# Optimization experiments

Hardware: AMD Instinct MI355X
Metric: run time of the kernel (lower is better)

Reference implementation:

```python
import jax, jax.numpy as jnp
import numpy as np


def setup_inputs() -> dict:
    key = jax.random.key(0)
    ks = jax.random.split(key, 15)
    B, r, d, h, na = 64, 64, 2048, 64, 256
    x = jax.random.normal(ks[0], (B, d, na), dtype=jnp.float32)
    L = jax.random.randint(ks[1], (B, 2, na), 0, 2).astype(jnp.float32)
    p = lambda i, shp: jax.random.normal(ks[i], shp, dtype=jnp.float32)
    return {
        "x": x, "L": L,
        "Aq": p(2, (r, d)), "Ak": p(3, (r, d)), "Av": p(4, (r, d)),
        "Aq1": p(5, (r, r)), "Ak1": p(6, (r, r)), "Av1": p(7, (r, r)),
        "Aq5": p(8, (r, r)), "Ak5": p(9, (r, r)), "Av5": p(10, (r, r)),
        "Ao": p(11, (r, r)), "Ao1": p(12, (r, r)), "Ao5": p(13, (h, r)),
    }


def reference(x, L, Aq, Ak, Av, Aq1, Ak1, Av1, Aq5, Ak5, Av5, Ao, Ao1, Ao5):
    B, d, na = x.shape
    # numNeighbors: count of L[:,0,:] >= 1 per batch, +1 -> [B,1,1]
    numN = jnp.sum((L[:, 0, :] >= 1.0).astype(jnp.float32), axis=1)[:, None, None] + 1.0
    scale = jnp.sqrt(numN)  # [B,1,1]

    def attn(M, Wq, Wk, Wv):
        # M: [B, f, na]; Wq/Wk/Wv: [r, f]
        Q = jax.nn.sigmoid(jnp.einsum('rf,bfn->bnr', Wq, M))  # [B,na,r]
        K = jax.nn.sigmoid(jnp.einsum('rf,bfn->brn', Wk, M))  # [B,r,na]
        V = jax.nn.sigmoid(jnp.einsum('rf,bfn->bnr', Wv, M))  # [B,na,r]
        A = jax.nn.softmax(jnp.einsum('bnr,brm->bnm', Q, K) / scale, axis=2)
        return jnp.einsum('bnm,bmr->brn', A, V)  # [B,r,na]

    o = attn(x, Aq, Ak, Av)
    M = jax.nn.silu(jnp.einsum('sr,brn->bsn', Ao, o))
    o = attn(M, Aq1, Ak1, Av1)
    M = jax.nn.silu(jnp.einsum('sr,brn->bsn', Ao1, o))
    o = attn(M, Aq5, Ak5, Av5)
    M = jax.nn.silu(jnp.einsum('hr,brn->bhn', Ao5, o))  # [B,h,na]

    blk = d // na  # rows per block (8)
    def diagvec(i):
        # kron(sum-of-squares, ones(1,2)) == repeat each element twice -> [B, 2*na]
        return jnp.repeat(jnp.sum(M[:, i * blk:(i + 1) * blk, :] ** 2, axis=1), 2, axis=1)

    M11, M12, M21, M22 = diagvec(0), diagvec(1), diagvec(2), diagvec(3)
    Mpp = jnp.sum(M[:, 4 * blk:, :] ** 2, axis=1)  # [B, na]

    # q = x[:, :4, :].transpose(1,2).reshape(B, 4*na) (agent-major ordering)
    q = jnp.transpose(x[:, :4, :], (0, 2, 1)).reshape(B, 4 * na)
    q1, q2 = q[:, :2 * na], q[:, 2 * na:]
    # Block matrix [[diag(M11), diag(M12)], [diag(M21), diag(M22)]] quadratic form,
    # computed without materializing the [B, 4na, 4na] matrix.
    quad = jnp.sum(M11 * q1 * q1 + M12 * q1 * q2 + M21 * q2 * q1 + M22 * q2 * q2,
                   axis=1, keepdims=True)
    return quad + jnp.sum(Mpp, axis=1, keepdims=True)  # [B, 1]
```

## Files before the change

kernel.cpp:

```cpp
#include <hip/hip_runtime.h>
#include <stdint.h>

typedef _Float16 f16;
typedef f16 f16x8 __attribute__((ext_vector_type(8)));
typedef float f32x4 __attribute__((ext_vector_type(4)));

#define MFMA(a,b,c) __builtin_amdgcn_mfma_f32_16x16x32_f16(a, b, c, 0, 0, 0)

__device__ __forceinline__ float sigmoidf_(float z) {
  return __builtin_amdgcn_rcpf(1.0f + __expf(-z));
}

__global__ void prep_kernel(const float* __restrict__ L,
    const float* __restrict__ Aq, const float* __restrict__ Ak, const float* __restrict__ Av,
    const float* __restrict__ Aq1, const float* __restrict__ Ak1, const float* __restrict__ Av1,
    const float* __restrict__ Aq5, const float* __restrict__ Ak5, const float* __restrict__ Av5,
    const float* __restrict__ Ao, const float* __restrict__ Ao1, const float* __restrict__ Ao5,
    float* __restrict__ scale, f16* __restrict__ Wcat, f16* __restrict__ Wsm,
    float* __restrict__ out)
{
  __shared__ float r4[4];
  int blk = blockIdx.x, t = threadIdx.x;
  if (blk < 64) {
    float v = (L[blk * 512 + t] >= 1.0f) ? 1.0f : 0.0f;
    #pragma unroll
    for (int off = 32; off; off >>= 1) v += __shfl_down(v, off);
    if ((t & 63) == 0) r4[t >> 6] = v;
    __syncthreads();
    if (t == 0) scale[blk] = sqrtf(r4[0] + r4[1] + r4[2] + r4[3] + 1.0f);
  } else if (blk < 160) {
    int base = (blk - 64) * 4096;
    for (int i = 0; i < 16; i++) {
      int idx = base + t + i * 256;
      int row = idx >> 11, col = idx & 2047;
      float v = (row < 64) ? Aq[row * 2048 + col]
              : (row < 128) ? Ak[(row - 64) * 2048 + col]
              : Av[(row - 128) * 2048 + col];
      Wcat[idx] = (f16)v;
    }
  } else if (blk < 169) {
    int j = blk - 160;
    const float* s = (j == 0) ? Aq1 : (j == 1) ? Ak1 : (j == 2) ? Av1 : (j == 3) ? Aq5
                   : (j == 4) ? Ak5 : (j == 5) ? Av5 : (j == 6) ? Ao : (j == 7) ? Ao1 : Ao5;
    for (int i = 0; i < 16; i++) { int idx = t + i * 256; Wsm[j * 4096 + idx] = (f16)s[idx]; }
  } else {
    if (t < 64) out[t] = 0.0f;
  }
}

__global__ __launch_bounds__(256, 4) void qkv1_kernel(const float* __restrict__ x,
    const f16* __restrict__ Wcat, f16* __restrict__ Qt, f16* __restrict__ Kt,
    f16* __restrict__ Vg)
{
  int rs = blockIdx.x, b = blockIdx.y, ng = blockIdx.z;
  int n0 = ng * 32, rbase = rs * 64;
  int t = threadIdx.x, lane = t & 63, w = t >> 6;
  int l15 = lane & 15, q = lane >> 4;
  __shared__ f16 xt[2][32 * 72];
  __shared__ f16 wt[2][64 * 72];
  f32x4 acc[2] = {};
  const float* xb = x + (size_t)b * 524288 + n0;
  int tn = t & 31, fg = t >> 5;

  int r0 = t >> 3,          c0 = t & 7;
  int r1 = (t + 256) >> 3,  c1 = (t + 256) & 7;
  const f16* pw0 = Wcat + (size_t)(rbase + r0) * 2048 + c0 * 8;
  const f16* pw1 = Wcat + (size_t)(rbase + r1) * 2048 + c1 * 8;
  const float* px = xb + (size_t)(fg * 8) * 256 + tn;

  float xa0, xa1, xa2, xa3, xa4, xa5, xa6, xa7;
  uint4 wr0, wr1;

#define LOAD_X(f0n) do {                                                        \
    const float* xp_ = px + (size_t)(f0n) * 256;                                \
    xa0 = xp_[0];    xa1 = xp_[256];  xa2 = xp_[512];  xa3 = xp_[768];          \
    xa4 = xp_[1024]; xa5 = xp_[1280]; xa6 = xp_[1536]; xa7 = xp_[1792];         \
  } while (0)

#define LOAD_W(f0n) do {                                                        \
    wr0 = *(const uint4*)(pw0 + (f0n)); wr1 = *(const uint4*)(pw1 + (f0n));     \
  } while (0)

#define WRITE_XW(buf) do {                                                      \
    f16x8 pk_;                                                                  \
    pk_[0] = (f16)xa0; pk_[1] = (f16)xa1; pk_[2] = (f16)xa2; pk_[3] = (f16)xa3; \
    pk_[4] = (f16)xa4; pk_[5] = (f16)xa5; pk_[6] = (f16)xa6; pk_[7] = (f16)xa7; \
    *(f16x8*)&xt[buf][tn * 72 + fg * 8] = pk_;                                  \
    f16* wb_ = &wt[buf][0];                                                     \
    *(uint4*)&wb_[r0 * 72 + c0 * 8] = wr0;                                      \
    *(uint4*)&wb_[r1 * 72 + c1 * 8] = wr1;                                      \
  } while (0)

  LOAD_X(0);
  LOAD_W(0);
  WRITE_XW(0);
  __syncthreads();

  int cur = 0;
  for (int f0 = 0; f0 < 2048; f0 += 64) {
    int nxt = cur ^ 1;
    bool more = (f0 + 64 < 2048);
    if (more) { LOAD_X(f0 + 64); LOAD_W(f0 + 64); }

    #pragma unroll
    for (int ks = 0; ks < 2; ks++) {
      int k0 = ks * 32 + q * 8;
      f16x8 af0 = *(const f16x8*)&xt[cur][l15 * 72 + k0];
      f16x8 af1 = *(const f16x8*)&xt[cur][(16 + l15) * 72 + k0];
      f16x8 bf  = *(const f16x8*)&wt[cur][(w * 16 + l15) * 72 + k0];
      acc[0] = MFMA(af0, bf, acc[0]);
      acc[1] = MFMA(af1, bf, acc[1]);
    }

    if (more) WRITE_XW(nxt);
    __syncthreads();
    cur = nxt;
  }
#undef LOAD_X
#undef LOAD_W
#undef WRITE_XW

  int rr = rbase + w * 16 + l15;
  #pragma unroll
  for (int nt = 0; nt < 2; nt++) {
    float s[4];
    #pragma unroll
    for (int reg = 0; reg < 4; reg++) s[reg] = sigmoidf_(acc[nt][reg]);
    int nbase = n0 + nt * 16 + q * 4;
    if (rr < 64) {
      #pragma unroll
      for (int reg = 0; reg < 4; reg++)
        Qt[(size_t)b * 16384 + (size_t)(nbase + reg) * 64 + rr] = (f16)s[reg];
    } else if (rr < 128) {
      #pragma unroll
      for (int reg = 0; reg < 4; reg++)
        Kt[(size_t)b * 16384 + (size_t)(nbase + reg) * 64 + (rr - 64)] = (f16)s[reg];
    } else {
      union { f16 h[4]; uint2 u; } pk;
      #pragma unroll
      for (int reg = 0; reg < 4; reg++) pk.h[reg] = (f16)s[reg];
      *(uint2*)(Vg + (size_t)b * 16384 + (size_t)(rr - 128) * 256 + nbase) = pk.u;
    }
  }
}

template<int LAYER>
__global__ __launch_bounds__(1024) void attnB_kernel(const float* __restrict__ x,
    const float* __restrict__ scale, const f16* __restrict__ Wsm,
    const f16* __restrict__ Qtg, const f16* __restrict__ Ktg, const f16* __restrict__ Vgg,
    const f16* __restrict__ Min, f16* __restrict__ Mout, float* __restrict__ out)
{
  int g = blockIdx.x, b = blockIdx.y, n0 = g * 64;
  int t = threadIdx.x, lane = t & 63, w = t >> 6;
  int l15 = lane & 15, q = lane >> 4;
  __shared__ f16 KT[256 * 72];
  __shared__ f16 SM[256 * 72];
  __shared__ f16 VM[64 * 264];
  __shared__ f16 QT[64 * 72];
  __shared__ f16 OT[64 * 72];
  __shared__ float denomS[64];

  float sinv = __builtin_amdgcn_rcpf(scale[b]);
  if (t < 64) denomS[t] = 0.0f;

  if (LAYER == 0) {
    if (t < 512) {
      const uint4* qs = (const uint4*)(Qtg + (size_t)b * 16384 + (size_t)n0 * 64);
      int n = t >> 3, c = t & 7; *(uint4*)&QT[n * 72 + c * 8] = qs[t];
    }
    const uint4* ks = (const uint4*)(Ktg + (size_t)b * 16384);
    const uint4* vs = (const uint4*)(Vgg + (size_t)b * 16384);
    #pragma unroll
    for (int i = 0; i < 2; i++) {
      int id = t + i * 1024;
      int m = id >> 3, c = id & 7;
      *(uint4*)&KT[m * 72 + c * 8] = ks[id];
      int r = id >> 5, c2 = id & 31;
      *(uint4*)&VM[r * 264 + c2 * 8] = vs[id];
    }
  } else {
    const uint4* ms = (const uint4*)(Min + (size_t)b * 16384);
    #pragma unroll
    for (int i = 0; i < 2; i++) {
      int id = t + i * 1024, m = id >> 3, c = id & 7;
      *(uint4*)&SM[m * 72 + c * 8] = ms[id];
    }
  }
  __syncthreads();

  const f16* Wq = Wsm + (size_t)(LAYER == 1 ? 0 : 3) * 4096;
  const f16* Wk = Wsm + (size_t)(LAYER == 1 ? 1 : 4) * 4096;
  const f16* Wv = Wsm + (size_t)(LAYER == 1 ? 2 : 5) * 4096;
  const f16* Wo = Wsm + (size_t)(LAYER == 0 ? 6 : (LAYER == 1 ? 7 : 8)) * 4096;

  if (LAYER > 0) {
    if (w < 8) {
      f16x8 bk[4][2];
      #pragma unroll
      for (int rt = 0; rt < 4; rt++) {
        bk[rt][0] = *(const f16x8*)(Wk + (rt * 16 + l15) * 64 + q * 8);
        bk[rt][1] = *(const f16x8*)(Wk + (rt * 16 + l15) * 64 + 32 + q * 8);
      }
      #pragma unroll
      for (int mi = 0; mi < 2; mi++) {
        int mt = w * 2 + mi;
        f16x8 a0 = *(const f16x8*)&SM[(mt * 16 + l15) * 72 + q * 8];
        f16x8 a1 = *(const f16x8*)&SM[(mt * 16 + l15) * 72 + 32 + q * 8];
        #pragma unroll
        for (int rt = 0; rt < 4; rt++) {
          f32x4 acc = {}; acc = MFMA(a0, bk[rt][0], acc); acc = MFMA(a1, bk[rt][1], acc);
          #pragma unroll
          for (int reg = 0; reg < 4; reg++)
            KT[(mt * 16 + q * 4 + reg) * 72 + rt * 16 + l15] = (f16)sigmoidf_(acc[reg]);
        }
      }
    } else {
      f16x8 av[4][2];
      #pragma unroll
      for (int rt = 0; rt < 4; rt++) {
        av[rt][0] = *(const f16x8*)(Wv + (rt * 16 + l15) * 64 + q * 8);
        av[rt][1] = *(const f16x8*)(Wv + (rt * 16 + l15) * 64 + 32 + q * 8);
      }
      #pragma unroll
      for (int mi = 0; mi < 2; mi++) {
        int mt = (w - 8) * 2 + mi;
        f16x8 b0 = *(const f16x8*)&SM[(mt * 16 + l15) * 72 + q * 8];
        f16x8 b1 = *(const f16x8*)&SM[(mt * 16 + l15) * 72 + 32 + q * 8];
        #pragma unroll
        for (int rt = 0; rt < 4; rt++) {
          f32x4 acc = {}; acc = MFMA(av[rt][0], b0, acc); acc = MFMA(av[rt][1], b1, acc);
          #pragma unroll
          for (int reg = 0; reg < 4; reg++)
            VM[(rt * 16 + q * 4 + reg) * 264 + mt * 16 + l15] = (f16)sigmoidf_(acc[reg]);
        }
      }
    }
    {
      int nt = w >> 2, rt = w & 3;
      f16x8 a0 = *(const f16x8*)&SM[(n0 + nt * 16 + l15) * 72 + q * 8];
      f16x8 a1 = *(const f16x8*)&SM[(n0 + nt * 16 + l15) * 72 + 32 + q * 8];
      f16x8 b0 = *(const f16x8*)(Wq + (rt * 16 + l15) * 64 + q * 8);
      f16x8 b1 = *(const f16x8*)(Wq + (rt * 16 + l15) * 64 + 32 + q * 8);
      f32x4 acc = {}; acc = MFMA(a0, b0, acc); acc = MFMA(a1, b1, acc);
      #pragma unroll
      for (int reg = 0; reg < 4; reg++)
        QT[(nt * 16 + q * 4 + reg) * 72 + rt * 16 + l15] = (f16)sigmoidf_(acc[reg]);
    }
    __syncthreads();
  }

  {
    int nt = w >> 2;
    f16x8 a0 = *(const f16x8*)&QT[(nt * 16 + l15) * 72 + q * 8];
    f16x8 a1 = *(const f16x8*)&QT[(nt * 16 + l15) * 72 + 32 + q * 8];
    float dsum[4] = {0.f, 0.f, 0.f, 0.f};
    #pragma unroll
    for (int mi = 0; mi < 4; mi++) {
      int mt = (w & 3) * 4 + mi;
      f16x8 b0 = *(const f16x8*)&KT[(mt * 16 + l15) * 72 + q * 8];
      f16x8 b1 = *(const f16x8*)&KT[(mt * 16 + l15) * 72 + 32 + q * 8];
      f32x4 acc = {}; acc = MFMA(a0, b0, acc); acc = MFMA(a1, b1, acc);
      #pragma unroll
      for (int reg = 0; reg < 4; reg++) {
        float e = __expf(acc[reg] * sinv);
        dsum[reg] += e;
        SM[(nt * 16 + q * 4 + reg) * 264 + mt * 16 + l15] = (f16)e;
      }
    }
    #pragma unroll
    for (int reg = 0; reg < 4; reg++) {
      #pragma unroll
      for (int mask = 1; mask < 16; mask <<= 1) dsum[reg] += __shfl_xor(dsum[reg], mask);
    }
    if (l15 == 0) {
      #pragma unroll
      for (int reg = 0; reg < 4; reg++) atomicAdd(&denomS[nt * 16 + q * 4 + reg], dsum[reg]);
    }
  }
  __syncthreads();

  {
    int nt = w >> 2, rt = w & 3;
    f32x4 oacc = {};
    #pragma unroll
    for (int kc = 0; kc < 8; kc++) {
      f16x8 af = *(const f16x8*)&SM[(nt * 16 + l15) * 264 + kc * 32 + q * 8];
      f16x8 bf = *(const f16x8*)&VM[(rt * 16 + l15) * 264 + kc * 32 + q * 8];
      oacc = MFMA(af, bf, oacc);
    }
    float rden[4];
    #pragma unroll
    for (int reg = 0; reg < 4; reg++)
      rden[reg] = __builtin_amdgcn_rcpf(denomS[nt * 16 + q * 4 + reg]);
    #pragma unroll
    for (int reg = 0; reg < 4; reg++) {
      int row = nt * 16 + q * 4 + reg;
      OT[row * 72 + rt * 16 + l15] = (f16)(oacc[reg] * rden[reg]);
    }
  }
  __syncthreads();

  f16* Mst = QT;
  {
    int nt = w >> 2, st = w & 3;
    f16x8 a0 = *(const f16x8*)&OT[(nt * 16 + l15) * 72 + q * 8];
    f16x8 a1 = *(const f16x8*)&OT[(nt * 16 + l15) * 72 + 32 + q * 8];
    f16x8 b0 = *(const f16x8*)(Wo + (st * 16 + l15) * 64 + q * 8);
    f16x8 b1 = *(const f16x8*)(Wo + (st * 16 + l15) * 64 + 32 + q * 8);
    f32x4 acc = {}; acc = MFMA(a0, b0, acc); acc = MFMA(a1, b1, acc);
    #pragma unroll
    for (int reg = 0; reg < 4; reg++) {
      float z = acc[reg];
      Mst[(nt * 16 + q * 4 + reg) * 64 + st * 16 + l15] = (f16)(z * sigmoidf_(z));
    }
  }
  __syncthreads();

  if (LAYER < 2) {
    if (t < 512) {
      int row = t >> 3, c = t & 7;
      *(uint4*)(Mout + (size_t)b * 16384 + (size_t)(n0 + row) * 64 + c * 8)
          = *(const uint4*)&Mst[row * 64 + c * 8];
    }
  } else {
    float contrib = 0.0f;
    if (t < 64) {
      int ntok = n0 + t;
      const f16* row = &Mst[t * 64];
      float d[4] = {0, 0, 0, 0}, pp = 0.0f;
      #pragma unroll
      for (int gg = 0; gg < 8; gg++) {
        f16x8 v = *(const f16x8*)(row + gg * 8);
        float ss = 0.0f;
        #pragma unroll
        for (int k = 0; k < 8; k++) { float f = (float)v[k]; ss += f * f; }
        if (gg < 4) d[gg] = ss; else pp += ss;
      }
      int np = ntok >> 1, c0 = (ntok & 1) * 2;
      const float* xb = x + (size_t)b * 524288 + (size_t)c0 * 256;
      float q1a = xb[np], q1b = xb[256 + np];
      float q2a = xb[128 + np], q2b = xb[384 + np];
      contrib = d[0] * (q1a * q1a + q1b * q1b)
              + (d[1] + d[2]) * (q1a * q2a + q1b * q2b)
              + d[3] * (q2a * q2a + q2b * q2b) + pp;
    }
    if (w == 0) {
      #pragma unroll
      for (int off = 32; off; off >>= 1) contrib += __shfl_down(contrib, off);
      if (lane == 0) atomicAdd(out + b, contrib);
    }
  }
}

extern "C" void kernel_launch(void* const* d_in, const int* in_sizes, int n_in,
                              void* d_out, int out_size, void* d_ws, size_t ws_size,
                              hipStream_t stream) {
  const float* x   = (const float*)d_in[0];
  const float* L   = (const float*)d_in[1];
  const float* Aq  = (const float*)d_in[2];
  const float* Ak  = (const float*)d_in[3];
  const float* Av  = (const float*)d_in[4];
  const float* Aq1 = (const float*)d_in[5];
  const float* Ak1 = (const float*)d_in[6];
  const float* Av1 = (const float*)d_in[7];
  const float* Aq5 = (const float*)d_in[8];
  const float* Ak5 = (const float*)d_in[9];
  const float* Av5 = (const float*)d_in[10];
  const float* Ao  = (const float*)d_in[11];
  const float* Ao1 = (const float*)d_in[12];
  const float* Ao5 = (const float*)d_in[13];

  char* ws = (char*)d_ws;
  float* scale = (float*)ws;
  f16* Wcat  = (f16*)(ws + 256);
  f16* Wsm   = (f16*)(ws + 786688);
  f16* Qtg   = (f16*)(ws + 860416);
  f16* Ktg   = (f16*)(ws + 2957568);
  f16* Vgg   = (f16*)(ws + 5054720);
  f16* MbufA = (f16*)(ws + 7151872);
  f16* MbufB = (f16*)(ws + 9249024);
  float* out = (float*)d_out;

  prep_kernel<<<170, 256, 0, stream>>>(L, Aq, Ak, Av, Aq1, Ak1, Av1,
                                       Aq5, Ak5, Av5, Ao, Ao1, Ao5, scale, Wcat, Wsm, out);
  qkv1_kernel<<<dim3(3, 64, 8), 256, 0, stream>>>(x, Wcat, Qtg, Ktg, Vgg);
  attnB_kernel<0><<<dim3(4, 64), 1024, 0, stream>>>(x, scale, Wsm, Qtg, Ktg, Vgg,
                                                    nullptr, MbufA, out);
  attnB_kernel<1><<<dim3(4, 64), 1024, 0, stream>>>(x, scale, Wsm, Qtg, Ktg, Vgg,
                                                    MbufA, MbufB, out);
  attnB_kernel<2><<<dim3(4, 64), 1024, 0, stream>>>(x, scale, Wsm, Qtg, Ktg, Vgg,
                                                    MbufB, nullptr, out);
}
```

Measured before the change: 296.2 us.

## Retile QKV projection so each block covers all 192 rows for 16 agents

```diff
diff --git a/kernel.cpp b/kernel.cpp
--- a/kernel.cpp
+++ b/kernel.cpp
@@ -52,81 +52,77 @@
     const f16* __restrict__ Wcat, f16* __restrict__ Qt, f16* __restrict__ Kt,
     f16* __restrict__ Vg)
 {
-  int rs = blockIdx.x, b = blockIdx.y, ng = blockIdx.z;
-  int n0 = ng * 32, rbase = rs * 64;
+  int ng = blockIdx.x, b = blockIdx.y;
+  int n0 = ng * 16;
   int t = threadIdx.x, lane = t & 63, w = t >> 6;
   int l15 = lane & 15, q = lane >> 4;
-  __shared__ f16 xt[2][32 * 72];
-  __shared__ f16 wt[2][64 * 72];
-  f32x4 acc[2] = {};
+  __shared__ f16 xt[2][16 * 40];
+  __shared__ f16 wt[2][192 * 36];
+  f32x4 acc[3] = {};
   const float* xb = x + (size_t)b * 524288 + n0;
-  int tn = t & 31, fg = t >> 5;
-
-  int r0 = t >> 3,          c0 = t & 7;
-  int r1 = (t + 256) >> 3,  c1 = (t + 256) & 7;
-  const f16* pw0 = Wcat + (size_t)(rbase + r0) * 2048 + c0 * 8;
-  const f16* pw1 = Wcat + (size_t)(rbase + r1) * 2048 + c1 * 8;
-  const float* px = xb + (size_t)(fg * 8) * 256 + tn;
-
-  float xa0, xa1, xa2, xa3, xa4, xa5, xa6, xa7;
-  uint4 wr0, wr1;
-
-#define LOAD_X(f0n) do {                                                        \
+
+  int fr = t >> 3, c2 = (t & 7) * 2;
+  const float* px = xb + (size_t)fr * 256 + c2;
+  int wrr0 = t >> 2,         wcc0 = t & 3;
+  int wrr1 = (t + 256) >> 2, wcc1 = (t + 256) & 3;
+  int wrr2 = (t + 512) >> 2, wcc2 = (t + 512) & 3;
+  const f16* pw0 = Wcat + (size_t)wrr0 * 2048 + wcc0 * 8;
+  const f16* pw1 = Wcat + (size_t)wrr1 * 2048 + wcc1 * 8;
+  const f16* pw2 = Wcat + (size_t)wrr2 * 2048 + wcc2 * 8;
+
+  float xa0, xa1;
+  uint4 wv0, wv1, wv2;
+
+#define LOAD_XW(f0n) do {                                                       \
     const float* xp_ = px + (size_t)(f0n) * 256;                                \
-    xa0 = xp_[0];    xa1 = xp_[256];  xa2 = xp_[512];  xa3 = xp_[768];          \
-    xa4 = xp_[1024]; xa5 = xp_[1280]; xa6 = xp_[1536]; xa7 = xp_[1792];         \
+    xa0 = xp_[0]; xa1 = xp_[1];                                                 \
+    wv0 = *(const uint4*)(pw0 + (f0n));                                         \
+    wv1 = *(const uint4*)(pw1 + (f0n));                                         \
+    wv2 = *(const uint4*)(pw2 + (f0n));                                         \
   } while (0)
 
-#define LOAD_W(f0n) do {                                                        \
-    wr0 = *(const uint4*)(pw0 + (f0n)); wr1 = *(const uint4*)(pw1 + (f0n));     \
+#define WRITE_XW(buf) do {                                                      \
+    xt[buf][c2 * 40 + fr]       = (f16)xa0;                                     \
+    xt[buf][(c2 + 1) * 40 + fr] = (f16)xa1;                                     \
+    f16* wb_ = &wt[buf][0];                                                     \
+    *(uint4*)&wb_[wrr0 * 36 + wcc0 * 8] = wv0;                                  \
+    *(uint4*)&wb_[wrr1 * 36 + wcc1 * 8] = wv1;                                  \
+    *(uint4*)&wb_[wrr2 * 36 + wcc2 * 8] = wv2;                                  \
   } while (0)
 
-#define WRITE_XW(buf) do {                                                      \
-    f16x8 pk_;                                                                  \
-    pk_[0] = (f16)xa0; pk_[1] = (f16)xa1; pk_[2] = (f16)xa2; pk_[3] = (f16)xa3; \
-    pk_[4] = (f16)xa4; pk_[5] = (f16)xa5; pk_[6] = (f16)xa6; pk_[7] = (f16)xa7; \
-    *(f16x8*)&xt[buf][tn * 72 + fg * 8] = pk_;                                  \
-    f16* wb_ = &wt[buf][0];                                                     \
-    *(uint4*)&wb_[r0 * 72 + c0 * 8] = wr0;                                      \
-    *(uint4*)&wb_[r1 * 72 + c1 * 8] = wr1;                                      \
-  } while (0)
-
-  LOAD_X(0);
-  LOAD_W(0);
+  LOAD_XW(0);
   WRITE_XW(0);
   __syncthreads();
 
   int cur = 0;
-  for (int f0 = 0; f0 < 2048; f0 += 64) {
+  for (int f0 = 0; f0 < 2048; f0 += 32) {
     int nxt = cur ^ 1;
-    bool more = (f0 + 64 < 2048);
-    if (more) { LOAD_X(f0 + 64); LOAD_W(f0 + 64); }
-
-    #pragma unroll
-    for (int ks = 0; ks < 2; ks++) {
-      int k0 = ks * 32 + q * 8;
-      f16x8 af0 = *(const f16x8*)&xt[cur][l15 * 72 + k0];
-      f16x8 af1 = *(const f16x8*)&xt[cur][(16 + l15) * 72 + k0];
-      f16x8 bf  = *(const f16x8*)&wt[cur][(w * 16 + l15) * 72 + k0];
-      acc[0] = MFMA(af0, bf, acc[0]);
-      acc[1] = MFMA(af1, bf, acc[1]);
+    bool more = (f0 + 32 < 2048);
+    if (more) LOAD_XW(f0 + 32);
+
+    {
+      f16x8 af = *(const f16x8*)&xt[cur][l15 * 40 + q * 8];
+      #pragma unroll
+      for (int j = 0; j < 3; j++) {
+        f16x8 bf = *(const f16x8*)&wt[cur][(w * 48 + j * 16 + l15) * 36 + q * 8];
+        acc[j] = MFMA(af, bf, acc[j]);
+      }
     }
 
     if (more) WRITE_XW(nxt);
     __syncthreads();
     cur = nxt;
   }
-#undef LOAD_X
-#undef LOAD_W
+#undef LOAD_XW
 #undef WRITE_XW
 
-  int rr = rbase + w * 16 + l15;
   #pragma unroll
-  for (int nt = 0; nt < 2; nt++) {
+  for (int j = 0; j < 3; j++) {
+    int rr = w * 48 + j * 16 + l15;
     float s[4];
     #pragma unroll
-    for (int reg = 0; reg < 4; reg++) s[reg] = sigmoidf_(acc[nt][reg]);
-    int nbase = n0 + nt * 16 + q * 4;
+    for (int reg = 0; reg < 4; reg++) s[reg] = sigmoidf_(acc[j][reg]);
+    int nbase = n0 + q * 4;
     if (rr < 64) {
       #pragma unroll
       for (int reg = 0; reg < 4; reg++)
@@ -383,7 +379,7 @@
 
   prep_kernel<<<170, 256, 0, stream>>>(L, Aq, Ak, Av, Aq1, Ak1, Av1,
                                        Aq5, Ak5, Av5, Ao, Ao1, Ao5, scale, Wcat, Wsm, out);
-  qkv1_kernel<<<dim3(3, 64, 8), 256, 0, stream>>>(x, Wcat, Qtg, Ktg, Vgg);
+  qkv1_kernel<<<dim3(16, 64), 256, 0, stream>>>(x, Wcat, Qtg, Ktg, Vgg);
   attnB_kernel<0><<<dim3(4, 64), 1024, 0, stream>>>(x, scale, Wsm, Qtg, Ktg, Vgg,
                                                     nullptr, MbufA, out);
   attnB_kernel<1><<<dim3(4, 64), 1024, 0, stream>>>(x, scale, Wsm, Qtg, Ktg, Vgg,
```

After: 341.8 us. 15.4% more time.
